# Kernel tuning notes

Hardware: AMD Instinct MI355X
Metric: run time of the kernel (lower is better)

The kernel has to match this reference:

```python
import jax, jax.numpy as jnp
import numpy as np

TIME_CONSTANT = 1.0
VM_THRESHOLD = 2.0
WINDOW = 100          # integration_window
AMPLITUDE = 1.0


def setup_inputs() -> dict:
    key = jax.random.key(0)
    # [B, T, H, W, C] positive drive so integrate-and-fire actually spikes
    inputs = jax.random.uniform(key, (4, 200, 64, 64, 8), dtype=jnp.float32)
    return {"inputs": inputs}


def _process_chunk(chunk):
    """Iterative integrate-and-fire on one time chunk [B, T, H, W, C].
    Each while-iteration extracts one spike per neuron (first threshold
    crossing of the running cumsum), resets the membrane, and zeroes the
    consumed input so the next cumsum restarts after the spike."""
    B, T = chunk.shape[0], chunk.shape[1]
    img = chunk.shape[2:]
    spikes0 = jnp.zeros((B,) + img + (T + 1,), chunk.dtype)
    vout0 = jnp.zeros_like(chunk)

    def body(state):
        ch, vout, spikes, _ = state
        V = jnp.cumsum(ch * TIME_CONSTANT, axis=1)            # membrane potential
        temp = jax.nn.relu(V - VM_THRESHOLD)
        has = jnp.any(temp > 0)                                # any neuron fires?
        ctemp = jnp.cumsum(temp, axis=1)                       # zero before first crossing
        tstar = jnp.sum((ctemp == 0).astype(jnp.int32), axis=1)  # [B,H,W,C] spike time (T => none)
        spikes_new = spikes + jax.nn.one_hot(tstar, T + 1, dtype=ch.dtype)
        rolled = jnp.roll(ctemp, 1, axis=1).at[:, 0].set(0.0)  # nonzero strictly after spike
        mask = rolled == 0
        vout_spk = jnp.where(mask, vout + V, 0.0)              # record V up to spike, reset after
        ch_spk = jnp.where(mask, 0.0, ch)                      # consume input up to spike
        # if no spikes this pass: accumulate residual V and stop (do-while break)
        vout_n = jnp.where(has, vout_spk, vout + V)
        ch_n = jnp.where(has, ch_spk, ch)
        spikes_n = jnp.where(has, spikes_new, spikes)
        return ch_n, vout_n, spikes_n, jnp.logical_not(has)

    def cond(state):
        return jnp.logical_not(state[3])

    state = (chunk, vout0, spikes0, jnp.array(False))
    _, vout, spikes, _ = jax.lax.while_loop(cond, body, state)
    return vout, spikes[..., :T]   # drop the 'no spike' bin


def reference(inputs):
    T = inputs.shape[1]
    sizes = [WINDOW] * (T // WINDOW) + ([T % WINDOW] if T % WINDOW else [])
    spike_chunks = []
    start = 0
    for s in sizes:  # small fixed chunk loop (structural, not a data dim)
        ch = inputs[:, start:start + s]
        start += s
        _, sp = _process_chunk(ch)
        spike_chunks.append(sp)
    spikes = jnp.concatenate(spike_chunks, axis=-1)   # [B, H, W, C, T]
    out = jnp.swapaxes(spikes, 1, -1)                 # [B, T, W, C, H] (as in source)
    if AMPLITUDE != 1.0:
        out = out * AMPLITUDE
    return out
```

## Files before the change

kernel.cpp:

```cpp
#include <hip/hip_runtime.h>
#include <stdint.h>

#define HWC    32768
#define NSLAB  8
#define TTOT   200
#define CHUNK  100

__global__ __launch_bounds__(256) void spike_bits(const float* __restrict__ x,
                                                  uint32_t* __restrict__ spk) {
    unsigned g    = blockIdx.x * 256u + threadIdx.x;
    unsigned slab = g >> 15;
    unsigned n    = g & (HWC - 1);
    unsigned b    = slab >> 1, ch = slab & 1u;
    const float* xp = x + (size_t)(b * TTOT + ch * CHUNK) * HWC + n;

    float acc = 0.0f;
    uint32_t w0 = 0u, w1 = 0u, w2 = 0u, w3 = 0u;
    uint32_t* wsel[1]; (void)wsel;

#define STEP(WREG, TB, K)                                         \
    do {                                                          \
        acc += v[K];                                              \
        if (acc > 2.0f) { WREG |= (1u << ((TB) + (K))); acc = 0.0f; } \
    } while (0)

#define GROUP8(WREG, TBASE)                                       \
    do {                                                          \
        float v[8];                                               \
        _Pragma("unroll")                                         \
        for (int k = 0; k < 8; ++k) v[k] = xp[(size_t)((TBASE) + k) * HWC]; \
        STEP(WREG, (TBASE) & 31, 0); STEP(WREG, (TBASE) & 31, 1); \
        STEP(WREG, (TBASE) & 31, 2); STEP(WREG, (TBASE) & 31, 3); \
        STEP(WREG, (TBASE) & 31, 4); STEP(WREG, (TBASE) & 31, 5); \
        STEP(WREG, (TBASE) & 31, 6); STEP(WREG, (TBASE) & 31, 7); \
    } while (0)

    GROUP8(w0,  0); GROUP8(w0,  8); GROUP8(w0, 16); GROUP8(w0, 24);
    GROUP8(w1, 32); GROUP8(w1, 40); GROUP8(w1, 48); GROUP8(w1, 56);
    GROUP8(w2, 64); GROUP8(w2, 72); GROUP8(w2, 80); GROUP8(w2, 88);
    {
        float v[4];
#pragma unroll
        for (int k = 0; k < 4; ++k) v[k] = xp[(size_t)(96 + k) * HWC];
        STEP(w3, 0, 0); STEP(w3, 0, 1); STEP(w3, 0, 2); STEP(w3, 0, 3);
    }
#undef GROUP8
#undef STEP

    uint32_t* sp = spk + ((size_t)slab << 17);
    sp[n]            = w0;
    sp[HWC + n]      = w1;
    sp[2u * HWC + n] = w2;
    sp[3u * HWC + n] = w3;
}

__global__ __launch_bounds__(512) void expand_bits(const uint32_t* __restrict__ spk,
                                                   float* __restrict__ out) {
    __shared__ uint32_t lds[2 * 2112];
    unsigned gid  = blockIdx.x;
    unsigned slab = gid >> 6;
    unsigned q    = (gid >> 4) & 3u;
    unsigned tile = gid & 15u;
    unsigned wc0  = tile * 32u;
    unsigned t0   = q * 25u;
    unsigned p0   = t0 >> 5;
    unsigned p1   = (t0 + 24u) >> 5;
    unsigned tid  = threadIdx.x;

    const uint32_t* sbase = spk + ((size_t)slab << 17);
#pragma unroll
    for (int it = 0; it < 8; ++it) {
        unsigned idx = it * 512u + tid;
        unsigned pl  = idx >> 11;
        unsigned r   = idx & 2047u;
        unsigned h   = r >> 5, wcl = r & 31u;
        unsigned tw  = pl ? p1 : p0;
        lds[pl * 2112u + h * 33u + wcl] =
            sbase[((size_t)tw << 15) + h * 512u + wc0 + wcl];
    }
    __syncthreads();

    unsigned wcl = tid >> 4;
    unsigned h0  = (tid & 15u) * 4u;
    uint32_t r0[4], r1[4];
#pragma unroll
    for (int k = 0; k < 4; ++k) {
        r0[k] = lds[(h0 + k) * 33u + wcl];
        r1[k] = lds[2112u + (h0 + k) * 33u + wcl];
    }

    unsigned b = slab >> 1, ch = slab & 1u;
    unsigned rbase = b * TTOT + ch * CHUNK;
    float4* o4 = (float4*)out;

#pragma unroll
    for (int j = 0; j < 25; ++j) {
        unsigned t   = t0 + j;
        unsigned sel = (t >> 5) != p0;
        unsigned bit = t & 31u;
        uint32_t a0 = sel ? r1[0] : r0[0];
        uint32_t a1 = sel ? r1[1] : r0[1];
        uint32_t a2 = sel ? r1[2] : r0[2];
        uint32_t a3 = sel ? r1[3] : r0[3];
        float4 v;
        v.x = (float)((a0 >> bit) & 1u);
        v.y = (float)((a1 >> bit) & 1u);
        v.z = (float)((a2 >> bit) & 1u);
        v.w = (float)((a3 >> bit) & 1u);
        o4[(size_t)(rbase + t) * 8192u + wc0 * 16u + tid] = v;
    }
}

__global__ __launch_bounds__(256) void spike_kernel_ip(const float* __restrict__ x,
                                                       uint8_t* __restrict__ spk) {
    unsigned g     = blockIdx.x * 256u + threadIdx.x;
    unsigned chunk = g >> 16;
    unsigned p     = g & 65535u;
    unsigned b     = p >> 14;
    unsigned i     = (p & 16383u) * 2u;
    unsigned t0    = b * TTOT + chunk * CHUNK;
    const float2* xp = (const float2*)(x + (size_t)t0 * HWC + i);
    uint8_t*      sp = spk + (size_t)t0 * 131072u + i;
    float a0 = 0.0f, a1 = 0.0f;
    for (int tb = 0; tb < CHUNK; tb += 4) {
        float2 v[4];
#pragma unroll
        for (int k = 0; k < 4; ++k) v[k] = xp[(size_t)k * (HWC / 2)];
        xp += 4 * (HWC / 2);
#pragma unroll
        for (int k = 0; k < 4; ++k) {
            a0 += v[k].x; a1 += v[k].y;
            unsigned s0 = 0u, s1 = 0u;
            if (a0 > 2.0f) { s0 = 1u; a0 = 0.0f; }
            if (a1 > 2.0f) { s1 = 1u; a1 = 0.0f; }
            *(uint16_t*)sp = (uint16_t)(s0 | (s1 << 8));
            sp += 131072u;
        }
    }
}

__global__ __launch_bounds__(512) void transpose_ip(float* __restrict__ out) {
    __shared__ uint32_t lds[64 * 129];
    unsigned region = blockIdx.x;
    unsigned tid = threadIdx.x;
    const uint32_t* in32 = (const uint32_t*)((const uint8_t*)out + (size_t)region * 131072u);
#pragma unroll
    for (int it = 0; it < 16; ++it) {
        unsigned idx = it * 512u + tid;
        unsigned h = idx >> 7, wq = idx & 127u;
        lds[h * 129u + wq] = in32[idx];
    }
    __syncthreads();
    float4* out4 = (float4*)out + (size_t)region * 8192u;
#pragma unroll
    for (int it = 0; it < 16; ++it) {
        unsigned f  = it * 512u + tid;
        unsigned wc = f >> 4;
        unsigned h0 = (f & 15u) << 2;
        unsigned wq = wc >> 2, sel = (wc & 3u) * 8u;
        float4 v;
        v.x = (float)((lds[(h0 + 0u) * 129u + wq] >> sel) & 1u);
        v.y = (float)((lds[(h0 + 1u) * 129u + wq] >> sel) & 1u);
        v.z = (float)((lds[(h0 + 2u) * 129u + wq] >> sel) & 1u);
        v.w = (float)((lds[(h0 + 3u) * 129u + wq] >> sel) & 1u);
        out4[f] = v;
    }
}

extern "C" void kernel_launch(void* const* d_in, const int* in_sizes, int n_in,
                              void* d_out, int out_size, void* d_ws, size_t ws_size,
                              hipStream_t stream) {
    (void)in_sizes; (void)n_in; (void)out_size;
    const float* x = (const float*)d_in[0];
    float* out = (float*)d_out;

    const size_t bit_bytes = (size_t)NSLAB * 4u * HWC * 4u;
    if (ws_size >= bit_bytes) {
        uint32_t* spk = (uint32_t*)d_ws;
        hipLaunchKernelGGL(spike_bits, dim3(1024), dim3(256), 0, stream, x, spk);
        hipLaunchKernelGGL(expand_bits, dim3(512), dim3(512), 0, stream, spk, out);
    } else {
        hipLaunchKernelGGL(spike_kernel_ip, dim3(512), dim3(256), 0, stream, x, (uint8_t*)out);
        hipLaunchKernelGGL(transpose_ip, dim3(NSLAB * CHUNK), dim3(512), 0, stream, out);
    }
}
```

Measured before the change: 183.6 us.

## Fuse spike integration and bit expansion into a single kernel via LDS

Replaces the two-kernel pipeline (spike bitmask to workspace, then expand/transpose to output) with one kernel. Each thread integrates two neurons with float2 loads, writes bitmasks into shared memory, then the block expands them to float output in the transposed layout. This removes the global bit-buffer round trip and a launch, and drops the fallback path. The cost is fewer total threads and a serial scan per block before stores, which may reduce latency hiding.

```diff
diff --git a/kernel.cpp b/kernel.cpp
--- a/kernel.cpp
+++ b/kernel.cpp
@@ -1,186 +1,113 @@
 #include <hip/hip_runtime.h>
 #include <stdint.h>
 
-#define HWC    32768
-#define NSLAB  8
-#define TTOT   200
-#define CHUNK  100
+#define HWC   32768
+#define TTOT  200
+#define CHUNK 100
 
-__global__ __launch_bounds__(256) void spike_bits(const float* __restrict__ x,
-                                                  uint32_t* __restrict__ spk) {
-    unsigned g    = blockIdx.x * 256u + threadIdx.x;
-    unsigned slab = g >> 15;
-    unsigned n    = g & (HWC - 1);
+__global__ __launch_bounds__(256) void spike_fused(const float* __restrict__ x,
+                                                   float* __restrict__ out) {
+    __shared__ uint32_t lds[4 * 544];
+
+    unsigned bid  = blockIdx.x;
+    unsigned slab = bid >> 6;
+    unsigned hh   = (bid >> 5) & 1u;
+    unsigned tile = bid & 31u;
     unsigned b    = slab >> 1, ch = slab & 1u;
-    const float* xp = x + (size_t)(b * TTOT + ch * CHUNK) * HWC + n;
+    unsigned h0   = hh * 32u;
+    unsigned wc0  = tile * 16u;
+    unsigned tid  = threadIdx.x;
 
-    float acc = 0.0f;
-    uint32_t w0 = 0u, w1 = 0u, w2 = 0u, w3 = 0u;
-    uint32_t* wsel[1]; (void)wsel;
+    {
+        unsigned hl = tid >> 3;
+        unsigned wq = tid & 7u;
+        unsigned n  = (h0 + hl) * 512u + wc0 + wq * 2u;
+        const float2* xp = (const float2*)x
+            + (((size_t)(b * TTOT + ch * CHUNK) * HWC + n) >> 1);
 
-#define STEP(WREG, TB, K)                                         \
-    do {                                                          \
-        acc += v[K];                                              \
-        if (acc > 2.0f) { WREG |= (1u << ((TB) + (K))); acc = 0.0f; } \
+        float a0 = 0.0f, a1 = 0.0f;
+        uint32_t wa[4] = {0u, 0u, 0u, 0u};
+        uint32_t wb[4] = {0u, 0u, 0u, 0u};
+
+#define STEP(TW, BB, K)                                                     \
+    do {                                                                    \
+        a0 += v[K].x;                                                       \
+        if (a0 > 2.0f) { wa[TW] |= (1u << ((BB) + (K))); a0 = 0.0f; }       \
+        a1 += v[K].y;                                                       \
+        if (a1 > 2.0f) { wb[TW] |= (1u << ((BB) + (K))); a1 = 0.0f; }       \
     } while (0)
 
-#define GROUP8(WREG, TBASE)                                       \
-    do {                                                          \
-        float v[8];                                               \
-        _Pragma("unroll")                                         \
-        for (int k = 0; k < 8; ++k) v[k] = xp[(size_t)((TBASE) + k) * HWC]; \
-        STEP(WREG, (TBASE) & 31, 0); STEP(WREG, (TBASE) & 31, 1); \
-        STEP(WREG, (TBASE) & 31, 2); STEP(WREG, (TBASE) & 31, 3); \
-        STEP(WREG, (TBASE) & 31, 4); STEP(WREG, (TBASE) & 31, 5); \
-        STEP(WREG, (TBASE) & 31, 6); STEP(WREG, (TBASE) & 31, 7); \
+#define GROUP8(TW, TBASE)                                                   \
+    do {                                                                    \
+        float2 v[8];                                                        \
+        _Pragma("unroll")                                                   \
+        for (int k = 0; k < 8; ++k)                                         \
+            v[k] = xp[(size_t)((TBASE) + k) * (HWC / 2)];                   \
+        STEP(TW, (TBASE) & 31, 0); STEP(TW, (TBASE) & 31, 1);               \
+        STEP(TW, (TBASE) & 31, 2); STEP(TW, (TBASE) & 31, 3);               \
+        STEP(TW, (TBASE) & 31, 4); STEP(TW, (TBASE) & 31, 5);               \
+        STEP(TW, (TBASE) & 31, 6); STEP(TW, (TBASE) & 31, 7);               \
     } while (0)
 
-    GROUP8(w0,  0); GROUP8(w0,  8); GROUP8(w0, 16); GROUP8(w0, 24);
-    GROUP8(w1, 32); GROUP8(w1, 40); GROUP8(w1, 48); GROUP8(w1, 56);
-    GROUP8(w2, 64); GROUP8(w2, 72); GROUP8(w2, 80); GROUP8(w2, 88);
-    {
-        float v[4];
+        GROUP8(0,  0); GROUP8(0,  8); GROUP8(0, 16); GROUP8(0, 24);
+        GROUP8(1, 32); GROUP8(1, 40); GROUP8(1, 48); GROUP8(1, 56);
+        GROUP8(2, 64); GROUP8(2, 72); GROUP8(2, 80); GROUP8(2, 88);
+        {
+            float2 v[4];
 #pragma unroll
-        for (int k = 0; k < 4; ++k) v[k] = xp[(size_t)(96 + k) * HWC];
-        STEP(w3, 0, 0); STEP(w3, 0, 1); STEP(w3, 0, 2); STEP(w3, 0, 3);
-    }
+            for (int k = 0; k < 4; ++k)
+                v[k] = xp[(size_t)(96 + k) * (HWC / 2)];
+            STEP(3, 0, 0); STEP(3, 0, 1); STEP(3, 0, 2); STEP(3, 0, 3);
+        }
 #undef GROUP8
 #undef STEP
 
-    uint32_t* sp = spk + ((size_t)slab << 17);
-    sp[n]            = w0;
-    sp[HWC + n]      = w1;
-    sp[2u * HWC + n] = w2;
-    sp[3u * HWC + n] = w3;
-}
-
-__global__ __launch_bounds__(512) void expand_bits(const uint32_t* __restrict__ spk,
-                                                   float* __restrict__ out) {
-    __shared__ uint32_t lds[2 * 2112];
-    unsigned gid  = blockIdx.x;
-    unsigned slab = gid >> 6;
-    unsigned q    = (gid >> 4) & 3u;
-    unsigned tile = gid & 15u;
-    unsigned wc0  = tile * 32u;
-    unsigned t0   = q * 25u;
-    unsigned p0   = t0 >> 5;
-    unsigned p1   = (t0 + 24u) >> 5;
-    unsigned tid  = threadIdx.x;
-
-    const uint32_t* sbase = spk + ((size_t)slab << 17);
+        unsigned lbase = hl * 17u + wq * 2u;
 #pragma unroll
-    for (int it = 0; it < 8; ++it) {
-        unsigned idx = it * 512u + tid;
-        unsigned pl  = idx >> 11;
-        unsigned r   = idx & 2047u;
-        unsigned h   = r >> 5, wcl = r & 31u;
-        unsigned tw  = pl ? p1 : p0;
-        lds[pl * 2112u + h * 33u + wcl] =
-            sbase[((size_t)tw << 15) + h * 512u + wc0 + wcl];
+        for (int tw = 0; tw < 4; ++tw) {
+            lds[tw * 544u + lbase]      = wa[tw];
+            lds[tw * 544u + lbase + 1u] = wb[tw];
+        }
     }
     __syncthreads();
 
-    unsigned wcl = tid >> 4;
-    unsigned h0  = (tid & 15u) * 4u;
-    uint32_t r0[4], r1[4];
+    unsigned idx  = tid & 127u;
+    unsigned half = tid >> 7;
+    unsigned wcl  = idx >> 3;
+    unsigned hl4  = (idx & 7u) * 4u;
+
+    uint32_t r[4][4];
 #pragma unroll
-    for (int k = 0; k < 4; ++k) {
-        r0[k] = lds[(h0 + k) * 33u + wcl];
-        r1[k] = lds[2112u + (h0 + k) * 33u + wcl];
-    }
+    for (int k = 0; k < 4; ++k)
+#pragma unroll
+        for (int tw = 0; tw < 4; ++tw)
+            r[k][tw] = lds[tw * 544u + (hl4 + k) * 17u + wcl];
 
-    unsigned b = slab >> 1, ch = slab & 1u;
     unsigned rbase = b * TTOT + ch * CHUNK;
-    float4* o4 = (float4*)out;
+    size_t   cbase = (size_t)(wc0 + wcl) * 16u + ((h0 + hl4) >> 2);
+    float4*  o4    = (float4*)out;
 
 #pragma unroll
-    for (int j = 0; j < 25; ++j) {
-        unsigned t   = t0 + j;
-        unsigned sel = (t >> 5) != p0;
-        unsigned bit = t & 31u;
-        uint32_t a0 = sel ? r1[0] : r0[0];
-        uint32_t a1 = sel ? r1[1] : r0[1];
-        uint32_t a2 = sel ? r1[2] : r0[2];
-        uint32_t a3 = sel ? r1[3] : r0[3];
-        float4 v;
-        v.x = (float)((a0 >> bit) & 1u);
-        v.y = (float)((a1 >> bit) & 1u);
-        v.z = (float)((a2 >> bit) & 1u);
-        v.w = (float)((a3 >> bit) & 1u);
-        o4[(size_t)(rbase + t) * 8192u + wc0 * 16u + tid] = v;
-    }
-}
-
-__global__ __launch_bounds__(256) void spike_kernel_ip(const float* __restrict__ x,
-                                                       uint8_t* __restrict__ spk) {
-    unsigned g     = blockIdx.x * 256u + threadIdx.x;
-    unsigned chunk = g >> 16;
-    unsigned p     = g & 65535u;
-    unsigned b     = p >> 14;
-    unsigned i     = (p & 16383u) * 2u;
-    unsigned t0    = b * TTOT + chunk * CHUNK;
-    const float2* xp = (const float2*)(x + (size_t)t0 * HWC + i);
-    uint8_t*      sp = spk + (size_t)t0 * 131072u + i;
-    float a0 = 0.0f, a1 = 0.0f;
-    for (int tb = 0; tb < CHUNK; tb += 4) {
-        float2 v[4];
-#pragma unroll
-        for (int k = 0; k < 4; ++k) v[k] = xp[(size_t)k * (HWC / 2)];
-        xp += 4 * (HWC / 2);
-#pragma unroll
-        for (int k = 0; k < 4; ++k) {
-            a0 += v[k].x; a1 += v[k].y;
-            unsigned s0 = 0u, s1 = 0u;
-            if (a0 > 2.0f) { s0 = 1u; a0 = 0.0f; }
-            if (a1 > 2.0f) { s1 = 1u; a1 = 0.0f; }
-            *(uint16_t*)sp = (uint16_t)(s0 | (s1 << 8));
-            sp += 131072u;
+    for (int tw = 0; tw < 4; ++tw) {
+        const int nj = (tw < 3) ? 16 : 2;
+        for (int j = 0; j < nj; ++j) {
+            unsigned bit = 2u * (unsigned)j + half;
+            unsigned t   = (unsigned)tw * 32u + bit;
+            float4 v;
+            v.x = (float)((r[0][tw] >> bit) & 1u);
+            v.y = (float)((r[1][tw] >> bit) & 1u);
+            v.z = (float)((r[2][tw] >> bit) & 1u);
+            v.w = (float)((r[3][tw] >> bit) & 1u);
+            o4[((size_t)(rbase + t) << 13) + cbase] = v;
         }
-    }
-}
-
-__global__ __launch_bounds__(512) void transpose_ip(float* __restrict__ out) {
-    __shared__ uint32_t lds[64 * 129];
-    unsigned region = blockIdx.x;
-    unsigned tid = threadIdx.x;
-    const uint32_t* in32 = (const uint32_t*)((const uint8_t*)out + (size_t)region * 131072u);
-#pragma unroll
-    for (int it = 0; it < 16; ++it) {
-        unsigned idx = it * 512u + tid;
-        unsigned h = idx >> 7, wq = idx & 127u;
-        lds[h * 129u + wq] = in32[idx];
-    }
-    __syncthreads();
-    float4* out4 = (float4*)out + (size_t)region * 8192u;
-#pragma unroll
-    for (int it = 0; it < 16; ++it) {
-        unsigned f  = it * 512u + tid;
-        unsigned wc = f >> 4;
-        unsigned h0 = (f & 15u) << 2;
-        unsigned wq = wc >> 2, sel = (wc & 3u) * 8u;
-        float4 v;
-        v.x = (float)((lds[(h0 + 0u) * 129u + wq] >> sel) & 1u);
-        v.y = (float)((lds[(h0 + 1u) * 129u + wq] >> sel) & 1u);
-        v.z = (float)((lds[(h0 + 2u) * 129u + wq] >> sel) & 1u);
-        v.w = (float)((lds[(h0 + 3u) * 129u + wq] >> sel) & 1u);
-        out4[f] = v;
     }
 }
 
 extern "C" void kernel_launch(void* const* d_in, const int* in_sizes, int n_in,
                               void* d_out, int out_size, void* d_ws, size_t ws_size,
                               hipStream_t stream) {
-    (void)in_sizes; (void)n_in; (void)out_size;
+    (void)in_sizes; (void)n_in; (void)out_size; (void)d_ws; (void)ws_size;
     const float* x = (const float*)d_in[0];
     float* out = (float*)d_out;
-
-    const size_t bit_bytes = (size_t)NSLAB * 4u * HWC * 4u;
-    if (ws_size >= bit_bytes) {
-        uint32_t* spk = (uint32_t*)d_ws;
-        hipLaunchKernelGGL(spike_bits, dim3(1024), dim3(256), 0, stream, x, spk);
-        hipLaunchKernelGGL(expand_bits, dim3(512), dim3(512), 0, stream, spk, out);
-    } else {
-        hipLaunchKernelGGL(spike_kernel_ip, dim3(512), dim3(256), 0, stream, x, (uint8_t*)out);
-        hipLaunchKernelGGL(transpose_ip, dim3(NSLAB * CHUNK), dim3(512), 0, stream, out);
-    }
+    hipLaunchKernelGGL(spike_fused, dim3(512), dim3(256), 0, stream, x, out);
 }
```

After: 195.1 us. 6.2% more time.

## Vectorize spike scan to four neurons per thread with double-buffered loads

Applied to the files above, without the earlier changes.

The spike-bit kernel now handles four adjacent neurons per thread using float4 loads, and writes its packed bits as uint4. Loads for the next eight timesteps are issued while the current eight are consumed, using two register buffers. The grid shrinks from 1024 to 256 blocks, so there are far fewer waves on the device to hide memory latency, and each thread holds more registers.

```diff
diff --git a/kernel.cpp b/kernel.cpp
--- a/kernel.cpp
+++ b/kernel.cpp
@@ -6,52 +6,71 @@
 #define TTOT   200
 #define CHUNK  100
 
-__global__ __launch_bounds__(256) void spike_bits(const float* __restrict__ x,
-                                                  uint32_t* __restrict__ spk) {
+__global__ __launch_bounds__(256) void spike_bits4(const float* __restrict__ x,
+                                                   uint32_t* __restrict__ spk) {
     unsigned g    = blockIdx.x * 256u + threadIdx.x;
-    unsigned slab = g >> 15;
-    unsigned n    = g & (HWC - 1);
+    unsigned slab = g >> 13;
+    unsigned n0   = (g & 8191u) * 4u;
     unsigned b    = slab >> 1, ch = slab & 1u;
-    const float* xp = x + (size_t)(b * TTOT + ch * CHUNK) * HWC + n;
-
-    float acc = 0.0f;
-    uint32_t w0 = 0u, w1 = 0u, w2 = 0u, w3 = 0u;
-    uint32_t* wsel[1]; (void)wsel;
-
-#define STEP(WREG, TB, K)                                         \
-    do {                                                          \
-        acc += v[K];                                              \
-        if (acc > 2.0f) { WREG |= (1u << ((TB) + (K))); acc = 0.0f; } \
+    const float4* xp = (const float4*)(x + (size_t)(b * TTOT + ch * CHUNK) * HWC + n0);
+
+    float a0 = 0.0f, a1 = 0.0f, a2 = 0.0f, a3 = 0.0f;
+    uint32_t w[4][4] = {{0u,0u,0u,0u},{0u,0u,0u,0u},{0u,0u,0u,0u},{0u,0u,0u,0u}};
+    float4 A[8], B[8], Tl[4];
+
+#define LOAD8(V, TBASE)                                                     \
+    do {                                                                    \
+        _Pragma("unroll")                                                   \
+        for (int k = 0; k < 8; ++k)                                         \
+            V[k] = xp[(size_t)((TBASE) + k) * (HWC / 4)];                   \
     } while (0)
 
-#define GROUP8(WREG, TBASE)                                       \
-    do {                                                          \
-        float v[8];                                               \
-        _Pragma("unroll")                                         \
-        for (int k = 0; k < 8; ++k) v[k] = xp[(size_t)((TBASE) + k) * HWC]; \
-        STEP(WREG, (TBASE) & 31, 0); STEP(WREG, (TBASE) & 31, 1); \
-        STEP(WREG, (TBASE) & 31, 2); STEP(WREG, (TBASE) & 31, 3); \
-        STEP(WREG, (TBASE) & 31, 4); STEP(WREG, (TBASE) & 31, 5); \
-        STEP(WREG, (TBASE) & 31, 6); STEP(WREG, (TBASE) & 31, 7); \
+#define CONS8(V, TBASE)                                                     \
+    do {                                                                    \
+        _Pragma("unroll")                                                   \
+        for (int k = 0; k < 8; ++k) {                                       \
+            const int tw = (TBASE) >> 5, bb = ((TBASE) & 31) + k;           \
+            a0 += V[k].x; if (a0 > 2.0f) { w[tw][0] |= (1u << bb); a0 = 0.0f; } \
+            a1 += V[k].y; if (a1 > 2.0f) { w[tw][1] |= (1u << bb); a1 = 0.0f; } \
+            a2 += V[k].z; if (a2 > 2.0f) { w[tw][2] |= (1u << bb); a2 = 0.0f; } \
+            a3 += V[k].w; if (a3 > 2.0f) { w[tw][3] |= (1u << bb); a3 = 0.0f; } \
+        }                                                                   \
     } while (0)
 
-    GROUP8(w0,  0); GROUP8(w0,  8); GROUP8(w0, 16); GROUP8(w0, 24);
-    GROUP8(w1, 32); GROUP8(w1, 40); GROUP8(w1, 48); GROUP8(w1, 56);
-    GROUP8(w2, 64); GROUP8(w2, 72); GROUP8(w2, 80); GROUP8(w2, 88);
+    LOAD8(A, 0);  LOAD8(B, 8);
+    CONS8(A, 0);  LOAD8(A, 16);
+    CONS8(B, 8);  LOAD8(B, 24);
+    CONS8(A, 16); LOAD8(A, 32);
+    CONS8(B, 24); LOAD8(B, 40);
+    CONS8(A, 32); LOAD8(A, 48);
+    CONS8(B, 40); LOAD8(B, 56);
+    CONS8(A, 48); LOAD8(A, 64);
+    CONS8(B, 56); LOAD8(B, 72);
+    CONS8(A, 64); LOAD8(A, 80);
+    CONS8(B, 72); LOAD8(B, 88);
+    CONS8(A, 80);
     {
-        float v[4];
-#pragma unroll
-        for (int k = 0; k < 4; ++k) v[k] = xp[(size_t)(96 + k) * HWC];
-        STEP(w3, 0, 0); STEP(w3, 0, 1); STEP(w3, 0, 2); STEP(w3, 0, 3);
-    }
-#undef GROUP8
-#undef STEP
+#pragma unroll
+        for (int k = 0; k < 4; ++k)
+            Tl[k] = xp[(size_t)(96 + k) * (HWC / 4)];
+    }
+    CONS8(B, 88);
+#pragma unroll
+    for (int k = 0; k < 4; ++k) {
+        a0 += Tl[k].x; if (a0 > 2.0f) { w[3][0] |= (1u << k); a0 = 0.0f; }
+        a1 += Tl[k].y; if (a1 > 2.0f) { w[3][1] |= (1u << k); a1 = 0.0f; }
+        a2 += Tl[k].z; if (a2 > 2.0f) { w[3][2] |= (1u << k); a2 = 0.0f; }
+        a3 += Tl[k].w; if (a3 > 2.0f) { w[3][3] |= (1u << k); a3 = 0.0f; }
+    }
+#undef LOAD8
+#undef CONS8
 
     uint32_t* sp = spk + ((size_t)slab << 17);
-    sp[n]            = w0;
-    sp[HWC + n]      = w1;
-    sp[2u * HWC + n] = w2;
-    sp[3u * HWC + n] = w3;
+#pragma unroll
+    for (int tw = 0; tw < 4; ++tw) {
+        uint4 o; o.x = w[tw][0]; o.y = w[tw][1]; o.z = w[tw][2]; o.w = w[tw][3];
+        *(uint4*)(sp + (size_t)tw * HWC + n0) = o;
+    }
 }
 
 __global__ __launch_bounds__(512) void expand_bits(const uint32_t* __restrict__ spk,
@@ -177,7 +196,7 @@
     const size_t bit_bytes = (size_t)NSLAB * 4u * HWC * 4u;
     if (ws_size >= bit_bytes) {
         uint32_t* spk = (uint32_t*)d_ws;
-        hipLaunchKernelGGL(spike_bits, dim3(1024), dim3(256), 0, stream, x, spk);
+        hipLaunchKernelGGL(spike_bits4, dim3(256), dim3(256), 0, stream, x, spk);
         hipLaunchKernelGGL(expand_bits, dim3(512), dim3(512), 0, stream, spk, out);
     } else {
         hipLaunchKernelGGL(spike_kernel_ip, dim3(512), dim3(256), 0, stream, x, (uint8_t*)out);
```

Result: no change. 181.3 us (-1.3%).

## Stream spike-kernel input through LDS with async global_load_lds ring buffer

Applied to the files above, without the earlier changes.

Replaces the register-batched loads in the spike-bit kernel with a 20-deep software pipeline of direct global-to-LDS loads (global_load_lds), waiting on vmcnt before each timestep and refilling the slot just consumed. The goal is to keep many loads in flight per thread to hide HBM latency on the serial integrate-and-fire recurrence without using registers. It adds 20KB of LDS per block, which can limit occupancy, and relies on hand-placed waitcnt and sched barriers being correct.

```diff
diff --git a/kernel.cpp b/kernel.cpp
--- a/kernel.cpp
+++ b/kernel.cpp
@@ -6,52 +6,64 @@
 #define TTOT   200
 #define CHUNK  100
 
-__global__ __launch_bounds__(256) void spike_bits(const float* __restrict__ x,
-                                                  uint32_t* __restrict__ spk) {
+__global__ __launch_bounds__(256) void spike_bits_async(const float* __restrict__ x,
+                                                        uint32_t* __restrict__ spk) {
+    __shared__ float lds[20 * 256];
+
     unsigned g    = blockIdx.x * 256u + threadIdx.x;
     unsigned slab = g >> 15;
-    unsigned n    = g & (HWC - 1);
+    unsigned n    = g & 32767u;
     unsigned b    = slab >> 1, ch = slab & 1u;
-    const float* xp = x + (size_t)(b * TTOT + ch * CHUNK) * HWC + n;
+    const float* xb = x + (size_t)(b * TTOT + ch * CHUNK) * HWC + n;
+
+    unsigned lane = threadIdx.x & 63u;
+    float*   lw   = &lds[(threadIdx.x >> 6) * 64u];
 
     float acc = 0.0f;
-    uint32_t w0 = 0u, w1 = 0u, w2 = 0u, w3 = 0u;
-    uint32_t* wsel[1]; (void)wsel;
+    uint32_t w[4] = {0u, 0u, 0u, 0u};
 
-#define STEP(WREG, TB, K)                                         \
-    do {                                                          \
-        acc += v[K];                                              \
-        if (acc > 2.0f) { WREG |= (1u << ((TB) + (K))); acc = 0.0f; } \
+#define GL(T, SLOT)                                                        \
+    __builtin_amdgcn_global_load_lds(                                      \
+        (const __attribute__((address_space(1))) void*)(xb + (size_t)(T) * HWC), \
+        (__attribute__((address_space(3))) void*)(lw + (SLOT) * 256u),     \
+        4, 0, 0)
+
+#define STC(T, SLOT, VN)                                                   \
+    do {                                                                   \
+        asm volatile("s_waitcnt vmcnt(" #VN ")" ::: "memory");             \
+        __builtin_amdgcn_sched_barrier(0);                                 \
+        float v = lw[(SLOT) * 256u + lane];                                \
+        acc += v;                                                          \
+        if (acc > 2.0f) { w[(T) >> 5] |= (1u << ((T) & 31)); acc = 0.0f; } \
     } while (0)
 
-#define GROUP8(WREG, TBASE)                                       \
-    do {                                                          \
-        float v[8];                                               \
-        _Pragma("unroll")                                         \
-        for (int k = 0; k < 8; ++k) v[k] = xp[(size_t)((TBASE) + k) * HWC]; \
-        STEP(WREG, (TBASE) & 31, 0); STEP(WREG, (TBASE) & 31, 1); \
-        STEP(WREG, (TBASE) & 31, 2); STEP(WREG, (TBASE) & 31, 3); \
-        STEP(WREG, (TBASE) & 31, 4); STEP(WREG, (TBASE) & 31, 5); \
-        STEP(WREG, (TBASE) & 31, 6); STEP(WREG, (TBASE) & 31, 7); \
-    } while (0)
+#define ST(T, SLOT) do { STC(T, SLOT, 19); GL((T) + 20, SLOT); } while (0)
+#define ROW5(T0, S0) ST(T0, S0); ST((T0)+1, (S0)+1); ST((T0)+2, (S0)+2); \
+                     ST((T0)+3, (S0)+3); ST((T0)+4, (S0)+4)
+#define ROW20(T0) ROW5(T0, 0); ROW5((T0)+5, 5); ROW5((T0)+10, 10); ROW5((T0)+15, 15)
 
-    GROUP8(w0,  0); GROUP8(w0,  8); GROUP8(w0, 16); GROUP8(w0, 24);
-    GROUP8(w1, 32); GROUP8(w1, 40); GROUP8(w1, 48); GROUP8(w1, 56);
-    GROUP8(w2, 64); GROUP8(w2, 72); GROUP8(w2, 80); GROUP8(w2, 88);
-    {
-        float v[4];
 #pragma unroll
-        for (int k = 0; k < 4; ++k) v[k] = xp[(size_t)(96 + k) * HWC];
-        STEP(w3, 0, 0); STEP(w3, 0, 1); STEP(w3, 0, 2); STEP(w3, 0, 3);
-    }
-#undef GROUP8
-#undef STEP
+    for (int t = 0; t < 20; ++t) GL(t, t);
 
-    uint32_t* sp = spk + ((size_t)slab << 17);
-    sp[n]            = w0;
-    sp[HWC + n]      = w1;
-    sp[2u * HWC + n] = w2;
-    sp[3u * HWC + n] = w3;
+    ROW20(0); ROW20(20); ROW20(40); ROW20(60);
+
+    STC(80,  0, 19); STC(81,  1, 18); STC(82,  2, 17); STC(83,  3, 16);
+    STC(84,  4, 15); STC(85,  5, 14); STC(86,  6, 13); STC(87,  7, 12);
+    STC(88,  8, 11); STC(89,  9, 10); STC(90, 10,  9); STC(91, 11,  8);
+    STC(92, 12,  7); STC(93, 13,  6); STC(94, 14,  5); STC(95, 15,  4);
+    STC(96, 16,  3); STC(97, 17,  2); STC(98, 18,  1); STC(99, 19,  0);
+
+#undef ROW20
+#undef ROW5
+#undef ST
+#undef STC
+#undef GL
+
+    uint32_t* sp = spk + ((size_t)slab << 17) + n;
+    sp[0]            = w[0];
+    sp[HWC]          = w[1];
+    sp[2u * HWC]     = w[2];
+    sp[3u * HWC]     = w[3];
 }
 
 __global__ __launch_bounds__(512) void expand_bits(const uint32_t* __restrict__ spk,
@@ -177,7 +189,7 @@
     const size_t bit_bytes = (size_t)NSLAB * 4u * HWC * 4u;
     if (ws_size >= bit_bytes) {
         uint32_t* spk = (uint32_t*)d_ws;
-        hipLaunchKernelGGL(spike_bits, dim3(1024), dim3(256), 0, stream, x, spk);
+        hipLaunchKernelGGL(spike_bits_async, dim3(1024), dim3(256), 0, stream, x, spk);
         hipLaunchKernelGGL(expand_bits, dim3(512), dim3(512), 0, stream, spk, out);
     } else {
         hipLaunchKernelGGL(spike_kernel_ip, dim3(512), dim3(256), 0, stream, x, (uint8_t*)out);
```

Measured after the change: 182.2 us. About the same (-0.8%).
